# Performance work log

Measured on AMD Instinct MI355X. Metric: run time of the kernel, lower is better.

The kernel has to match this reference:

```python
import jax, jax.numpy as jnp
import numpy as np

N, E, C, H = 20000, 320000, 128, 8
DH = C // H
CUTOFF = 5.0
LN_EPS = 1e-5


def _xavier(k, fan_in, fan_out):
    lim = np.sqrt(6.0 / (fan_in + fan_out))
    return jax.random.uniform(k, (fan_in, fan_out), jnp.float32, -lim, lim)


def setup_inputs() -> dict:
    key = jax.random.key(0)
    ks = jax.random.split(key, 24)
    s = jax.random.normal(ks[0], (N, 1, C), jnp.float32)
    v = 0.1 * jax.random.normal(ks[1], (N, 3, C), jnp.float32)
    dir_ij = jax.random.normal(ks[2], (E, 3), jnp.float32)
    dir_ij = dir_ij / (jnp.linalg.norm(dir_ij, axis=-1, keepdims=True) + 1e-9)
    d_ij = jax.random.uniform(ks[3], (E,), jnp.float32, 0.0, CUTOFF)
    r_ij = 0.5 * jax.random.normal(ks[4], (E, C), jnp.float32)
    edge_index = jax.random.randint(ks[5], (2, E), 0, N, jnp.int64 if jax.config.jax_enable_x64 else jnp.int32)
    zb = lambda n: jnp.zeros((n,), jnp.float32)
    return {
        's': s, 'v': v, 'dir_ij': dir_ij, 'd_ij': d_ij, 'r_ij': r_ij,
        'edge_index': edge_index,
        'ln_g': jnp.ones((C,), jnp.float32), 'ln_b': zb(C),
        'Wq': _xavier(ks[6], C, C), 'bq': zb(C),
        'Wk': _xavier(ks[7], C, C), 'bk': zb(C),
        'Wg1': _xavier(ks[8], C, C), 'bg1': zb(C),
        'Wg2': _xavier(ks[9], C, 3 * C), 'bg2': zb(3 * C),
        'Wv1': _xavier(ks[10], C, C), 'bv1': zb(C),
        'Wv2': _xavier(ks[11], C, 3 * C), 'bv2': zb(3 * C),
        'Wre': _xavier(ks[12], C, C), 'bre': zb(C),
        'Wra': _xavier(ks[13], C, 3 * C), 'bra': zb(3 * C),
    }


def _layernorm(x, g, b):
    m = jnp.mean(x, axis=-1, keepdims=True)
    var = jnp.mean((x - m) ** 2, axis=-1, keepdims=True)
    return (x - m) * jax.lax.rsqrt(var + LN_EPS) * g + b


def _cosine_cutoff(d):
    return 0.5 * (jnp.cos(d * (np.pi / CUTOFF)) + 1.0) * (d < CUTOFF).astype(d.dtype)


def _segment_softmax(logits, seg, n):
    # logits: [E, H], seg: [E]
    m = jax.ops.segment_max(logits, seg, num_segments=n)
    m = jnp.where(jnp.isfinite(m), m, 0.0)
    e = jnp.exp(logits - m[seg])
    z = jax.ops.segment_sum(e, seg, num_segments=n)
    return e / (z[seg] + 1e-16)


def reference(s, v, dir_ij, d_ij, r_ij, edge_index,
              ln_g, ln_b, Wq, bq, Wk, bk, Wg1, bg1, Wg2, bg2,
              Wv1, bv1, Wv2, bv2, Wre, bre, Wra, bra):
    src, dst = edge_index[0], edge_index[1]  # PyG: x_j = x[src], x_i = x[dst]
    s_ln = _layernorm(s, ln_g, ln_b)          # [N,1,C]
    s2 = s_ln[:, 0, :]                         # [N,C]

    q = (s2 @ Wq + bq).reshape(N, H, DH)
    k = (s2 @ Wk + bk).reshape(N, H, DH)
    x3 = jax.nn.silu(s2 @ Wg1 + bg1) @ Wg2 + bg2   # gamma_s -> [N,3C]
    val = jax.nn.silu(s2 @ Wv1 + bv1) @ Wv2 + bv2  # gamma_v -> [N,3C]
    r_attn = jax.nn.silu(r_ij @ Wre + bre).reshape(E, H, DH)
    r_proj = r_ij @ Wra + bra                      # [E,3C]

    # attention logits and segment softmax over destination nodes
    alpha = jnp.einsum('ehd,ehd->eh', q[dst] * k[src], r_attn) if False else jnp.sum(q[dst] * k[src] * r_attn, axis=-1)  # [E,H]
    attn = _segment_softmax(alpha, dst, N)         # [E,H]

    sea = (attn[:, :, None] * val[src].reshape(E, H, 3 * DH)).reshape(E, 3 * C)
    saa = r_proj * x3[src] * _cosine_cutoff(d_ij)[:, None]
    msg = saa + sea                                # [E,3C]
    o_s, o_d, o_v = jnp.split(msg, 3, axis=-1)     # each [E,C]

    su = jax.ops.segment_sum(o_s, dst, num_segments=N)   # [N,C]
    v_msg = dir_ij[:, :, None] * o_d[:, None, :] + o_v[:, None, :] * v[src]  # [E,3,C]
    vu = jax.ops.segment_sum(v_msg, dst, num_segments=N)  # [N,3,C]

    s_out = s_ln + su[:, None, :]
    v_out = v + vu
    return s_out, v_out, r_ij  # last_layer=True returns f_ij unchanged
```

## Files before the change

kernel.cpp:

```cpp
#include <hip/hip_runtime.h>
#include <cstdint>
#include <cstddef>

#define N_NODES 20000
#define N_EDGES 320000

typedef __attribute__((ext_vector_type(8))) short short8;
typedef __attribute__((ext_vector_type(4))) float floatx4;

__device__ __forceinline__ unsigned short f2bf(float f){
  union { float f; unsigned int i; } v; v.f = f;
  unsigned int u = v.i;
  return (unsigned short)((u + 0x7FFFu + ((u >> 16) & 1u)) >> 16);
}
__device__ __forceinline__ float bf2f(unsigned short u){
  union { unsigned int i; float f; } v; v.i = ((unsigned int)u) << 16; return v.f;
}
__device__ __forceinline__ float siluf(float x){ return x / (1.f + __expf(-x)); }
__device__ __forceinline__ short8 ld_frag16(const unsigned short* p){
  uint4 u = *(const uint4*)p;
  return *(short8*)&u;
}
__device__ __forceinline__ int clampi(int x, int lo, int hi){ return min(max(x, lo), hi); }

__global__ void k_pack(const float* Wq, const float* Wk,
                       const float* Wg1, const float* Wv1,
                       const float* Wg2, const float* Wv2,
                       const float* Wre, const float* Wra,
                       const float* bq, const float* bk,
                       const float* bg1, const float* bv1,
                       const float* bg2, const float* bv2,
                       const float* bre, const float* bra,
                       unsigned short* B1p, unsigned short* Wg2p, unsigned short* Wv2p,
                       unsigned short* Wep,
                       float* bias1, float* biasg2, float* biasv2, float* biase,
                       int* hist)
{
  int tid = blockIdx.x * blockDim.x + threadIdx.x;
  if (tid < 229376){
    int idx, region;
    if (tid < 65536){ region = 0; idx = tid; }
    else if (tid < 114688){ region = 1; idx = tid - 65536; }
    else if (tid < 163840){ region = 2; idx = tid - 114688; }
    else { region = 3; idx = tid - 163840; }
    int j = idx & 7, lane = (idx >> 3) & 63, kk = (idx >> 9) & 3, c = idx >> 11;
    int k = kk*32 + (lane >> 4)*8 + j;
    int n = c*16 + (lane & 15);
    if (region == 0){
      float v = (n < 128) ? Wq[k*128 + n]
              : (n < 256) ? Wk[k*128 + n - 128]
              : (n < 384) ? Wg1[k*128 + n - 256]
              : Wv1[k*128 + n - 384];
      B1p[idx] = f2bf(v);
    } else if (region == 1){ Wg2p[idx] = f2bf(Wg2[k*384 + n]); }
    else if (region == 2){ Wv2p[idx] = f2bf(Wv2[k*384 + n]); }
    else {
      float v = (n < 128) ? Wre[k*128 + n] : Wra[k*384 + n - 128];
      Wep[idx] = f2bf(v);
    }
  }
  if (tid < 512){
    bias1[tid] = tid<128 ? bq[tid] : tid<256 ? bk[tid-128] : tid<384 ? bg1[tid-256] : bv1[tid-384];
    biase[tid] = tid<128 ? bre[tid] : bra[tid-128];
  }
  if (tid < 384){ biasg2[tid] = bg2[tid]; biasv2[tid] = bv2[tid]; }
  if (tid < N_NODES) hist[tid] = 0;
}

__global__ void k_ln(const float* s_in, const float* v_in, const float* g, const float* b,
                     unsigned short* s2b, unsigned short* vt)
{
  int wid = threadIdx.x >> 6, lane = threadIdx.x & 63;
  int n = blockIdx.x*4 + wid;
  if (n >= N_NODES) return;
  const float* row = s_in + (size_t)n*128;
  float2 xv = *(const float2*)(row + lane*2);
  float x0 = xv.x, x1 = xv.y;
  float s = x0 + x1, ss = x0*x0 + x1*x1;
  for (int m = 1; m <= 32; m <<= 1){ s += __shfl_xor(s, m); ss += __shfl_xor(ss, m); }
  float mean = s * (1.f/128.f);
  float var = ss * (1.f/128.f) - mean*mean;
  float rs = rsqrtf(var + 1e-5f);
  int ch = lane*2;
  float y0 = (x0-mean)*rs*g[ch]   + b[ch];
  float y1 = (x1-mean)*rs*g[ch+1] + b[ch+1];
  ushort2 ov; ov.x = f2bf(y0); ov.y = f2bf(y1);
  *(ushort2*)(s2b + (size_t)n*128 + ch) = ov;

  float2 va = *(const float2*)(v_in + ((size_t)n*3 + 0)*128 + ch);
  float2 vb = *(const float2*)(v_in + ((size_t)n*3 + 1)*128 + ch);
  float2 vc = *(const float2*)(v_in + ((size_t)n*3 + 2)*128 + ch);
  uint4 wv;
  wv.x = (unsigned int)f2bf(va.x) | ((unsigned int)f2bf(vb.x) << 16);
  wv.y = (unsigned int)f2bf(vc.x);
  wv.z = (unsigned int)f2bf(va.y) | ((unsigned int)f2bf(vb.y) << 16);
  wv.w = (unsigned int)f2bf(vc.y);
  *(uint4*)(vt + (size_t)n*512 + (size_t)ch*4) = wv;
}

__global__ void k_hist(const int* ei, int* hist){
  int e = blockIdx.x*blockDim.x + threadIdx.x;
  if (e < N_EDGES){
    int d = clampi(ei[N_EDGES + e], 0, N_NODES-1);
    atomicAdd(&hist[d], 1);
  }
}

__global__ void k_scan(const int* hist, int* row_start, int* cursor){
  __shared__ int wsum[17];
  __shared__ int carry_s;
  int tid = threadIdx.x, lane = tid & 63, wid = tid >> 6;
  if (tid == 0) carry_s = 0;
  __syncthreads();
  for (int base = 0; base < N_NODES; base += 1024){
    int i = base + tid;
    int v = (i < N_NODES) ? hist[i] : 0;
    int incl = v;
    for (int off = 1; off < 64; off <<= 1){
      int t = __shfl_up(incl, off);
      if (lane >= off) incl += t;
    }
    if (lane == 63) wsum[wid] = incl;
    __syncthreads();
    if (tid == 0){
      int acc = carry_s;
      for (int w2 = 0; w2 < 16; w2++){ int t = wsum[w2]; wsum[w2] = acc; acc += t; }
      wsum[16] = acc;
    }
    __syncthreads();
    int excl = wsum[wid] + incl - v;
    if (i < N_NODES){ row_start[i] = excl; cursor[i] = excl; }
    __syncthreads();
    if (tid == 0) carry_s = wsum[16];
    __syncthreads();
  }
  if (threadIdx.x == 0) row_start[N_NODES] = carry_s;
}

__global__ void k_scatter(const int* ei, const float* dir_ij, const float* d_ij,
                          int* cursor, int* perm_s, int* src_s, float* dird_s){
  int e = blockIdx.x*blockDim.x + threadIdx.x;
  if (e < N_EDGES){
    int d = clampi(ei[N_EDGES + e], 0, N_NODES-1);
    int pos = clampi(atomicAdd(&cursor[d], 1), 0, N_EDGES-1);
    perm_s[pos] = e;
    src_s[pos] = clampi(ei[e], 0, N_NODES-1);
    float4 dd;
    dd.x = dir_ij[(size_t)e*3 + 0];
    dd.y = dir_ij[(size_t)e*3 + 1];
    dd.z = dir_ij[(size_t)e*3 + 2];
    dd.w = d_ij[e];
    *(float4*)(dird_s + (size_t)pos*4) = dd;
  }
}

__global__ void __launch_bounds__(256) k_ngemm1(const unsigned short* s2b, const unsigned short* B1p, const float* bias1,
                        unsigned short* q_b, unsigned short* k_b, unsigned short* h1_b, unsigned short* h2_b)
{
  int wid = threadIdx.x >> 6, lane = threadIdx.x & 63;
  int tile = blockIdx.x*4 + wid;
  if (tile >= N_NODES/16) return;
  int l15 = lane & 15, q = lane >> 4;
  int n0 = tile*16;
  const unsigned short* arow = s2b + (size_t)(n0 + l15)*128 + q*8;
  short8 af[4];
  for (int kk = 0; kk < 4; kk++) af[kk] = ld_frag16(arow + kk*32);
  for (int c = 0; c < 32; c++){
    floatx4 acc = {0.f,0.f,0.f,0.f};
    const unsigned short* bp = B1p + (size_t)(c*4)*512 + lane*8;
    for (int kk = 0; kk < 4; kk++){
      short8 bf = ld_frag16(bp + kk*512);
      acc = __builtin_amdgcn_mfma_f32_16x16x32_bf16(af[kk], bf, acc, 0, 0, 0);
    }
    int col = c*16 + l15;
    float bias = bias1[col];
    unsigned short* dst; int cc;
    if      (c < 8){  dst = q_b;  cc = col; }
    else if (c < 16){ dst = k_b;  cc = col - 128; }
    else if (c < 24){ dst = h1_b; cc = col - 256; }
    else            { dst = h2_b; cc = col - 384; }
    bool act = (c >= 16);
    for (int r = 0; r < 4; r++){
      float vv = acc[r] + bias;
      if (act) vv = siluf(vv);
      int node = n0 + q*4 + r;
      dst[(size_t)node*128 + cc] = f2bf(vv);
    }
  }
}

__global__ void __launch_bounds__(256) k_ngemm2(const unsigned short* h1_b, const unsigned short* h2_b,
                        const unsigned short* Wg2p, const unsigned short* Wv2p,
                        const float* biasg2, const float* biasv2,
                        unsigned short* xv_b)
{
  int wid = threadIdx.x >> 6, lane = threadIdx.x & 63;
  int tile = blockIdx.x*4 + wid;
  if (tile >= N_NODES/16) return;
  int l15 = lane & 15, q = lane >> 4;
  int n0 = tile*16;
  for (int ph = 0; ph < 2; ph++){
    const unsigned short* srcm = ph ? h2_b : h1_b;
    const unsigned short* Wp   = ph ? Wv2p : Wg2p;
    const float* bs            = ph ? biasv2 : biasg2;
    const unsigned short* arow = srcm + (size_t)(n0 + l15)*128 + q*8;
    short8 af[4];
    for (int kk = 0; kk < 4; kk++) af[kk] = ld_frag16(arow + kk*32);
    for (int c = 0; c < 24; c++){
      floatx4 acc = {0.f,0.f,0.f,0.f};
      const unsigned short* bp = Wp + (size_t)(c*4)*512 + lane*8;
      for (int kk = 0; kk < 4; kk++){
        short8 bf = ld_frag16(bp + kk*512);
        acc = __builtin_amdgcn_mfma_f32_16x16x32_bf16(af[kk], bf, acc, 0, 0, 0);
      }
      int col = c*16 + l15;
      float bias = bs[col];
      for (int r = 0; r < 4; r++){
        float vv = acc[r] + bias;
        int node = n0 + q*4 + r;
        xv_b[(((size_t)node*384 + col) << 1) + ph] = f2bf(vv);
      }
    }
  }
}

__global__ void __launch_bounds__(256) k_alpha(const float* r_ij, const unsigned short* q_b, const unsigned short* k_b,
                       const unsigned short* Wep, const float* biase,
                       const int* row_start, const int* perm_s, const int* src_s,
                       float* alpha_s, float* stats_s, float* r_out)
{
  int wid = threadIdx.x >> 6, lane = threadIdx.x & 63;
  int n = blockIdx.x*4 + wid;
  int l15 = lane & 15, q = lane >> 4;
  int rs = clampi(row_start[n], 0, N_EDGES);
  int re = clampi(row_start[n+1], rs, N_EDGES);
  if (re <= rs) return;

  float m_run[8], z_run[8];
  #pragma unroll
  for (int h = 0; h < 8; h++){ m_run[h] = -1e30f; z_run[h] = 0.f; }

  for (int c0 = rs; c0 < re; c0 += 16){
    int iA = min(c0 + l15, re-1);
    bool validA = (c0 + l15 < re);
    int pA = clampi(perm_s[iA], 0, N_EDGES-1);
    const float* ar = r_ij + (size_t)pA*128 + q*8;
    float*       wr = r_out + (size_t)pA*128 + q*8;
    short8 af[4];
    for (int kk = 0; kk < 4; kk++){
      float4 a0 = *(const float4*)(ar + kk*32);
      float4 a1 = *(const float4*)(ar + kk*32 + 4);
      if (validA){ *(float4*)(wr + kk*32) = a0; *(float4*)(wr + kk*32 + 4) = a1; }
      short8 f;
      f[0]=(short)f2bf(a0.x); f[1]=(short)f2bf(a0.y); f[2]=(short)f2bf(a0.z); f[3]=(short)f2bf(a0.w);
      f[4]=(short)f2bf(a1.x); f[5]=(short)f2bf(a1.y); f[6]=(short)f2bf(a1.z); f[7]=(short)f2bf(a1.w);
      af[kk] = f;
    }
    int sv[4]; int er_[4]; bool vr[4];
    for (int r = 0; r < 4; r++){
      int e = c0 + q*4 + r;
      vr[r] = (e < re);
      int ec = min(e, re-1);
      er_[r] = e;
      sv[r] = clampi(src_s[ec], 0, N_NODES-1);
    }
    for (int c = 0; c < 8; c++){
      floatx4 acc = {0.f,0.f,0.f,0.f};
      const unsigned short* bp = Wep + (size_t)(c*4)*512 + lane*8;
      for (int kk = 0; kk < 4; kk++){
        short8 bf = ld_frag16(bp + kk*512);
        acc = __builtin_amdgcn_mfma_f32_16x16x32_bf16(af[kk], bf, acc, 0, 0, 0);
      }
      float bias = biase[c*16 + l15];
      float qv = bf2f(q_b[(size_t)n*128 + c*16 + l15]);
      float t0[4];
      for (int r = 0; r < 4; r++){
        float kvv = bf2f(k_b[(size_t)sv[r]*128 + c*16 + l15]);
        t0[r] = siluf(acc[r] + bias) * qv * kvv;
      }
      for (int m = 1; m <= 8; m <<= 1)
        for (int r = 0; r < 4; r++) t0[r] += __shfl_xor(t0[r], m);
      if (l15 == 0){
        for (int r = 0; r < 4; r++)
          if (vr[r]) alpha_s[(size_t)er_[r]*8 + c] = t0[r];
      }
      for (int r = 0; r < 4; r++){
        if (vr[r]){
          float t = t0[r];
          float mn = fmaxf(m_run[c], t);
          z_run[c] = z_run[c]*__expf(m_run[c]-mn) + __expf(t-mn);
          m_run[c] = mn;
        }
      }
    }
  }
  for (int h = 0; h < 8; h++){
    float mo = m_run[h], zo = z_run[h];
    for (int m = 16; m <= 32; m <<= 1){
      float m2 = __shfl_xor(mo, m), z2 = __shfl_xor(zo, m);
      float mn = fmaxf(mo, m2);
      zo = zo*__expf(mo-mn) + z2*__expf(m2-mn);
      mo = mn;
    }
    m_run[h] = mo; z_run[h] = zo;
  }
  if (lane == 0){
    for (int h = 0; h < 8; h++){
      stats_s[(size_t)n*16 + h]     = m_run[h];
      stats_s[(size_t)n*16 + 8 + h] = 1.f / (z_run[h] + 1e-16f);
    }
  }
}

__global__ void __launch_bounds__(256) k_msg(const float* s_in, const float* v_in,
                     const float* r_ij,
                     const float* ln_g, const float* ln_b,
                     const unsigned short* xv_b, const unsigned short* vt_b,
                     const unsigned short* Wep, const float* biase,
                     const int* row_start, const int* perm_s, const int* src_s,
                     const float* dird_s, const float* alpha_s, const float* stats_s,
                     float* out_s, float* out_v)
{
  int wid = threadIdx.x >> 6, lane = threadIdx.x & 63;
  int n = blockIdx.x*4 + wid;
  int l15 = lane & 15, q = lane >> 4;
  int rs = clampi(row_start[n], 0, N_EDGES);
  int re = clampi(row_start[n+1], rs, N_EDGES);

  float accS[2] = {0.f, 0.f};
  float accV[6] = {0.f,0.f,0.f,0.f,0.f,0.f};

  int lh = lane & 7;
  float mh = stats_s[(size_t)n*16 + lh];
  float zi = stats_s[(size_t)n*16 + 8 + lh];

  for (int c0 = rs; c0 < re; c0 += 16){
    int iA = min(c0 + l15, re-1);
    int pA = clampi(perm_s[iA], 0, N_EDGES-1);
    const float* ar = r_ij + (size_t)pA*128 + q*8;
    short8 af[4];
    for (int kk = 0; kk < 4; kk++){
      float4 a0 = *(const float4*)(ar + kk*32);
      float4 a1 = *(const float4*)(ar + kk*32 + 4);
      short8 f;
      f[0]=(short)f2bf(a0.x); f[1]=(short)f2bf(a0.y); f[2]=(short)f2bf(a0.z); f[3]=(short)f2bf(a0.w);
      f[4]=(short)f2bf(a1.x); f[5]=(short)f2bf(a1.y); f[6]=(short)f2bf(a1.z); f[7]=(short)f2bf(a1.w);
      af[kk] = f;
    }

    int sv[4]; int er_[4]; bool vr[4]; float cc[4], dv0[4], dv1[4], dv2[4];
    for (int r = 0; r < 4; r++){
      int e = c0 + q*4 + r;
      vr[r] = (e < re);
      int ec = min(e, re-1);
      er_[r] = ec;
      sv[r] = clampi(src_s[ec], 0, N_NODES-1);
      float4 dd = *(const float4*)(dird_s + (size_t)ec*4);
      cc[r] = (vr[r] && dd.w < 5.0f) ? 0.5f*(__cosf(dd.w*0.6283185307179587f) + 1.f) : 0.f;
      dv0[r] = dd.x; dv1[r] = dd.y; dv2[r] = dd.z;
    }

    float at4[4] = {0.f,0.f,0.f,0.f};
    for (int c = 0; c < 24; c++){
      if (c % 3 == 0){
        int h = c / 3;
        float mhc = __shfl(mh, h);
        float zic = __shfl(zi, h);
        for (int r = 0; r < 4; r++)
          at4[r] = vr[r] ? __expf(alpha_s[(size_t)er_[r]*8 + h] - mhc) * zic : 0.f;
      }
      floatx4 acc = {0.f,0.f,0.f,0.f};
      const unsigned short* bp = Wep + (size_t)((8+c)*4)*512 + lane*8;
      for (int kk = 0; kk < 4; kk++){
        short8 bf = ld_frag16(bp + kk*512);
        acc = __builtin_amdgcn_mfma_f32_16x16x32_bf16(af[kk], bf, acc, 0, 0, 0);
      }
      float bias = biase[128 + c*16 + l15];
      float msg[4];
      for (int r = 0; r < 4; r++){
        unsigned int xv = *(const unsigned int*)(xv_b + (((size_t)sv[r]*384 + c*16 + l15) << 1));
        float xvf = bf2f((unsigned short)(xv & 0xffffu));
        float vvf = bf2f((unsigned short)(xv >> 16));
        msg[r] = (acc[r] + bias) * xvf * cc[r] + at4[r] * vvf;
      }
      if (c < 8){
        float s4 = msg[0]+msg[1]+msg[2]+msg[3];
        s4 += __shfl_xor(s4, 16); s4 += __shfl_xor(s4, 32);
        if (q == (c & 3)) accS[c >> 2] += s4;
      } else if (c < 16){
        int b = c - 8;
        float p0 = msg[0]*dv0[0] + msg[1]*dv0[1] + msg[2]*dv0[2] + msg[3]*dv0[3];
        float p1 = msg[0]*dv1[0] + msg[1]*dv1[1] + msg[2]*dv1[2] + msg[3]*dv1[3];
        float p2 = msg[0]*dv2[0] + msg[1]*dv2[1] + msg[2]*dv2[2] + msg[3]*dv2[3];
        p0 += __shfl_xor(p0, 16); p0 += __shfl_xor(p0, 32);
        p1 += __shfl_xor(p1, 16); p1 += __shfl_xor(p1, 32);
        p2 += __shfl_xor(p2, 16); p2 += __shfl_xor(p2, 32);
        if (q == (b & 3)){
          accV[(b >> 2)*3 + 0] += p0;
          accV[(b >> 2)*3 + 1] += p1;
          accV[(b >> 2)*3 + 2] += p2;
        }
      } else {
        int b = c - 16;
        float p0 = 0.f, p1 = 0.f, p2 = 0.f;
        for (int r = 0; r < 4; r++){
          uint2 vv = *(const uint2*)(vt_b + (((size_t)sv[r]*128 + b*16 + l15) << 2));
          p0 += msg[r] * bf2f((unsigned short)(vv.x & 0xffffu));
          p1 += msg[r] * bf2f((unsigned short)(vv.x >> 16));
          p2 += msg[r] * bf2f((unsigned short)(vv.y & 0xffffu));
        }
        p0 += __shfl_xor(p0, 16); p0 += __shfl_xor(p0, 32);
        p1 += __shfl_xor(p1, 16); p1 += __shfl_xor(p1, 32);
        p2 += __shfl_xor(p2, 16); p2 += __shfl_xor(p2, 32);
        if (q == (b & 3)){
          accV[(b >> 2)*3 + 0] += p0;
          accV[(b >> 2)*3 + 1] += p1;
          accV[(b >> 2)*3 + 2] += p2;
        }
      }
    }
  }

  {
    int ch0 = q*16 + l15, ch1 = 64 + q*16 + l15;
    float x0 = s_in[(size_t)n*128 + ch0];
    float x1 = s_in[(size_t)n*128 + ch1];
    float sm = x0 + x1, ssq = x0*x0 + x1*x1;
    for (int m = 1; m <= 32; m <<= 1){ sm += __shfl_xor(sm, m); ssq += __shfl_xor(ssq, m); }
    float mean = sm * (1.f/128.f);
    float var = ssq * (1.f/128.f) - mean*mean;
    float rsv = rsqrtf(var + 1e-5f);
    float y0 = (x0-mean)*rsv*ln_g[ch0] + ln_b[ch0];
    float y1 = (x1-mean)*rsv*ln_g[ch1] + ln_b[ch1];
    out_s[(size_t)n*128 + ch0] = y0 + accS[0];
    out_s[(size_t)n*128 + ch1] = y1 + accS[1];
  }
  for (int t = 0; t < 6; t++){
    int b = (t/3)*4 + q;
    int a = t - (t/3)*3;
    int ch = b*16 + l15;
    size_t idx = ((size_t)n*3 + a)*128 + ch;
    out_v[idx] = v_in[idx] + accV[t];
  }
}

extern "C" void kernel_launch(void* const* d_in, const int* in_sizes, int n_in,
                              void* d_out, int out_size, void* d_ws, size_t ws_size,
                              hipStream_t stream)
{
  const float* s_in   = (const float*)d_in[0];
  const float* v_in   = (const float*)d_in[1];
  const float* dir_ij = (const float*)d_in[2];
  const float* d_ij   = (const float*)d_in[3];
  const float* r_ij   = (const float*)d_in[4];
  const int*   ei     = (const int*)d_in[5];
  const float* ln_g   = (const float*)d_in[6];
  const float* ln_b   = (const float*)d_in[7];
  const float* Wq  = (const float*)d_in[8];
  const float* bq  = (const float*)d_in[9];
  const float* Wk  = (const float*)d_in[10];
  const float* bk  = (const float*)d_in[11];
  const float* Wg1 = (const float*)d_in[12];
  const float* bg1 = (const float*)d_in[13];
  const float* Wg2 = (const float*)d_in[14];
  const float* bg2 = (const float*)d_in[15];
  const float* Wv1 = (const float*)d_in[16];
  const float* bv1 = (const float*)d_in[17];
  const float* Wv2 = (const float*)d_in[18];
  const float* bv2 = (const float*)d_in[19];
  const float* Wre = (const float*)d_in[20];
  const float* bre = (const float*)d_in[21];
  const float* Wra = (const float*)d_in[22];
  const float* bra = (const float*)d_in[23];

  float* out_s = (float*)d_out;
  float* out_v = out_s + (size_t)N_NODES*128;
  float* out_r = out_v + (size_t)N_NODES*384;

  char* w = (char*)d_ws;
  size_t off = 0;
  auto alloc = [&](size_t bytes) -> void* {
    void* p = w + off;
    off = (off + bytes + 255) & ~(size_t)255;
    return p;
  };
  char* reg0 = (char*)alloc((size_t)N_EDGES*8*4);
  unsigned short* h1_b  = (unsigned short*)reg0;
  unsigned short* h2_b  = (unsigned short*)(reg0 + (size_t)N_NODES*128*2);
  float* alpha_s        = (float*)reg0;
  unsigned short* xv_b  = (unsigned short*)alloc((size_t)N_NODES*384*2*2);
  unsigned short* s2b   = xv_b;
  unsigned short* q_b   = (unsigned short*)alloc((size_t)N_NODES*128*2);
  unsigned short* k_b   = (unsigned short*)alloc((size_t)N_NODES*128*2);
  unsigned short* vt_b  = (unsigned short*)alloc((size_t)N_NODES*128*4*2);
  float* dird_s  = (float*)alloc((size_t)N_EDGES*4*4);
  float* stats_s = (float*)alloc((size_t)N_NODES*16*4);
  unsigned short* B1p   = (unsigned short*)alloc(65536*2);
  unsigned short* Wg2p  = (unsigned short*)alloc(49152*2);
  unsigned short* Wv2p  = (unsigned short*)alloc(49152*2);
  unsigned short* Wep   = (unsigned short*)alloc(65536*2);
  float* bias1  = (float*)alloc(512*4);
  float* biasg2 = (float*)alloc(384*4);
  float* biasv2 = (float*)alloc(384*4);
  float* biase  = (float*)alloc(512*4);
  int* hist      = (int*)alloc((size_t)N_NODES*4);
  int* row_start = (int*)alloc((size_t)(N_NODES+1)*4);
  int* cursor    = (int*)alloc((size_t)N_NODES*4);
  int* perm_s    = (int*)alloc((size_t)N_EDGES*4);
  int* src_s     = (int*)alloc((size_t)N_EDGES*4);

  k_pack<<<896, 256, 0, stream>>>(Wq, Wk, Wg1, Wv1, Wg2, Wv2, Wre, Wra,
                                  bq, bk, bg1, bv1, bg2, bv2, bre, bra,
                                  B1p, Wg2p, Wv2p, Wep,
                                  bias1, biasg2, biasv2, biase, hist);
  k_ln<<<5000, 256, 0, stream>>>(s_in, v_in, ln_g, ln_b, s2b, vt_b);
  k_hist<<<1250, 256, 0, stream>>>(ei, hist);
  k_scan<<<1, 1024, 0, stream>>>(hist, row_start, cursor);
  k_scatter<<<1250, 256, 0, stream>>>(ei, dir_ij, d_ij, cursor, perm_s, src_s, dird_s);
  k_ngemm1<<<313, 256, 0, stream>>>(s2b, B1p, bias1, q_b, k_b, h1_b, h2_b);
  k_ngemm2<<<313, 256, 0, stream>>>(h1_b, h2_b, Wg2p, Wv2p, biasg2, biasv2, xv_b);
  k_alpha<<<5000, 256, 0, stream>>>(r_ij, q_b, k_b, Wep, biase, row_start, perm_s, src_s,
                                    alpha_s, stats_s, out_r);
  k_msg<<<5000, 256, 0, stream>>>(s_in, v_in, r_ij, ln_g, ln_b,
                                  xv_b, vt_b, Wep, biase,
                                  row_start, perm_s, src_s, dird_s, alpha_s, stats_s,
                                  out_s, out_v);
}
```

Before: 1.021 ms.

## Cache bf16 edge features in sorted order and re-layout gathered node table

k_alpha now also writes a bf16 copy of r_ij in destination-sorted order, and k_msg reads it contiguously instead of re-gathering the fp32 rows through perm_s and converting them again. This halves the edge-feature bytes read in k_msg and removes the random gather, at the cost of an extra write pass and an 82 MB workspace buffer. The xv_b table is re-laid out so the 24 column chunks per lane are contiguous, which lets k_msg fetch four chunks per source node with one 16-byte load instead of many 4-byte gathers. The fallback path depends on the workspace size check.

```diff
diff --git a/kernel.cpp b/kernel.cpp
--- a/kernel.cpp
+++ b/kernel.cpp
@@ -218,13 +218,14 @@
       for (int r = 0; r < 4; r++){
         float vv = acc[r] + bias;
         int node = n0 + q*4 + r;
-        xv_b[(((size_t)node*384 + col) << 1) + ph] = f2bf(vv);
-      }
-    }
-  }
-}
-
-__global__ void __launch_bounds__(256) k_alpha(const float* r_ij, const unsigned short* q_b, const unsigned short* k_b,
+        xv_b[((((size_t)node*16 + l15)*24 + c) << 1) + ph] = f2bf(vv);
+      }
+    }
+  }
+}
+
+__global__ void __launch_bounds__(256) k_alpha(const float* r_ij, unsigned short* r_srt, int use_srt,
+                       const unsigned short* q_b, const unsigned short* k_b,
                        const unsigned short* Wep, const float* biase,
                        const int* row_start, const int* perm_s, const int* src_s,
                        float* alpha_s, float* stats_s, float* r_out)
@@ -246,6 +247,7 @@
     int pA = clampi(perm_s[iA], 0, N_EDGES-1);
     const float* ar = r_ij + (size_t)pA*128 + q*8;
     float*       wr = r_out + (size_t)pA*128 + q*8;
+    unsigned short* wsrt = r_srt + (size_t)iA*128 + q*8;
     short8 af[4];
     for (int kk = 0; kk < 4; kk++){
       float4 a0 = *(const float4*)(ar + kk*32);
@@ -255,6 +257,7 @@
       f[0]=(short)f2bf(a0.x); f[1]=(short)f2bf(a0.y); f[2]=(short)f2bf(a0.z); f[3]=(short)f2bf(a0.w);
       f[4]=(short)f2bf(a1.x); f[5]=(short)f2bf(a1.y); f[6]=(short)f2bf(a1.z); f[7]=(short)f2bf(a1.w);
       af[kk] = f;
+      if (use_srt && validA) *(short8*)(wsrt + kk*32) = f;
     }
     int sv[4]; int er_[4]; bool vr[4];
     for (int r = 0; r < 4; r++){
@@ -313,7 +316,7 @@
 }
 
 __global__ void __launch_bounds__(256) k_msg(const float* s_in, const float* v_in,
-                     const float* r_ij,
+                     const float* r_ij, const unsigned short* r_srt, int use_srt,
                      const float* ln_g, const float* ln_b,
                      const unsigned short* xv_b, const unsigned short* vt_b,
                      const unsigned short* Wep, const float* biase,
@@ -336,19 +339,25 @@
 
   for (int c0 = rs; c0 < re; c0 += 16){
     int iA = min(c0 + l15, re-1);
-    int pA = clampi(perm_s[iA], 0, N_EDGES-1);
-    const float* ar = r_ij + (size_t)pA*128 + q*8;
     short8 af[4];
-    for (int kk = 0; kk < 4; kk++){
-      float4 a0 = *(const float4*)(ar + kk*32);
-      float4 a1 = *(const float4*)(ar + kk*32 + 4);
-      short8 f;
-      f[0]=(short)f2bf(a0.x); f[1]=(short)f2bf(a0.y); f[2]=(short)f2bf(a0.z); f[3]=(short)f2bf(a0.w);
-      f[4]=(short)f2bf(a1.x); f[5]=(short)f2bf(a1.y); f[6]=(short)f2bf(a1.z); f[7]=(short)f2bf(a1.w);
-      af[kk] = f;
+    if (use_srt){
+      const unsigned short* ar = r_srt + (size_t)iA*128 + q*8;
+      for (int kk = 0; kk < 4; kk++) af[kk] = ld_frag16(ar + kk*32);
+    } else {
+      int pA = clampi(perm_s[iA], 0, N_EDGES-1);
+      const float* ar = r_ij + (size_t)pA*128 + q*8;
+      for (int kk = 0; kk < 4; kk++){
+        float4 a0 = *(const float4*)(ar + kk*32);
+        float4 a1 = *(const float4*)(ar + kk*32 + 4);
+        short8 f;
+        f[0]=(short)f2bf(a0.x); f[1]=(short)f2bf(a0.y); f[2]=(short)f2bf(a0.z); f[3]=(short)f2bf(a0.w);
+        f[4]=(short)f2bf(a1.x); f[5]=(short)f2bf(a1.y); f[6]=(short)f2bf(a1.z); f[7]=(short)f2bf(a1.w);
+        af[kk] = f;
+      }
     }
 
     int sv[4]; int er_[4]; bool vr[4]; float cc[4], dv0[4], dv1[4], dv2[4];
+    #pragma unroll
     for (int r = 0; r < 4; r++){
       int e = c0 + q*4 + r;
       vr[r] = (e < re);
@@ -361,61 +370,75 @@
     }
 
     float at4[4] = {0.f,0.f,0.f,0.f};
-    for (int c = 0; c < 24; c++){
-      if (c % 3 == 0){
-        int h = c / 3;
-        float mhc = __shfl(mh, h);
-        float zic = __shfl(zi, h);
-        for (int r = 0; r < 4; r++)
-          at4[r] = vr[r] ? __expf(alpha_s[(size_t)er_[r]*8 + h] - mhc) * zic : 0.f;
-      }
-      floatx4 acc = {0.f,0.f,0.f,0.f};
-      const unsigned short* bp = Wep + (size_t)((8+c)*4)*512 + lane*8;
-      for (int kk = 0; kk < 4; kk++){
-        short8 bf = ld_frag16(bp + kk*512);
-        acc = __builtin_amdgcn_mfma_f32_16x16x32_bf16(af[kk], bf, acc, 0, 0, 0);
-      }
-      float bias = biase[128 + c*16 + l15];
-      float msg[4];
-      for (int r = 0; r < 4; r++){
-        unsigned int xv = *(const unsigned int*)(xv_b + (((size_t)sv[r]*384 + c*16 + l15) << 1));
-        float xvf = bf2f((unsigned short)(xv & 0xffffu));
-        float vvf = bf2f((unsigned short)(xv >> 16));
-        msg[r] = (acc[r] + bias) * xvf * cc[r] + at4[r] * vvf;
-      }
-      if (c < 8){
-        float s4 = msg[0]+msg[1]+msg[2]+msg[3];
-        s4 += __shfl_xor(s4, 16); s4 += __shfl_xor(s4, 32);
-        if (q == (c & 3)) accS[c >> 2] += s4;
-      } else if (c < 16){
-        int b = c - 8;
-        float p0 = msg[0]*dv0[0] + msg[1]*dv0[1] + msg[2]*dv0[2] + msg[3]*dv0[3];
-        float p1 = msg[0]*dv1[0] + msg[1]*dv1[1] + msg[2]*dv1[2] + msg[3]*dv1[3];
-        float p2 = msg[0]*dv2[0] + msg[1]*dv2[1] + msg[2]*dv2[2] + msg[3]*dv2[3];
-        p0 += __shfl_xor(p0, 16); p0 += __shfl_xor(p0, 32);
-        p1 += __shfl_xor(p1, 16); p1 += __shfl_xor(p1, 32);
-        p2 += __shfl_xor(p2, 16); p2 += __shfl_xor(p2, 32);
-        if (q == (b & 3)){
-          accV[(b >> 2)*3 + 0] += p0;
-          accV[(b >> 2)*3 + 1] += p1;
-          accV[(b >> 2)*3 + 2] += p2;
+    #pragma unroll 1
+    for (int gc = 0; gc < 6; gc++){
+      uint4 Xr0 = *(const uint4*)(xv_b + ((((size_t)sv[0]*16 + l15)*24 + gc*4) << 1));
+      uint4 Xr1 = *(const uint4*)(xv_b + ((((size_t)sv[1]*16 + l15)*24 + gc*4) << 1));
+      uint4 Xr2 = *(const uint4*)(xv_b + ((((size_t)sv[2]*16 + l15)*24 + gc*4) << 1));
+      uint4 Xr3 = *(const uint4*)(xv_b + ((((size_t)sv[3]*16 + l15)*24 + gc*4) << 1));
+      #pragma unroll
+      for (int j = 0; j < 4; j++){
+        int c = gc*4 + j;
+        if (c % 3 == 0){
+          int h = c / 3;
+          float mhc = __shfl(mh, h);
+          float zic = __shfl(zi, h);
+          #pragma unroll
+          for (int r = 0; r < 4; r++)
+            at4[r] = vr[r] ? __expf(alpha_s[(size_t)er_[r]*8 + h] - mhc) * zic : 0.f;
         }
-      } else {
-        int b = c - 16;
-        float p0 = 0.f, p1 = 0.f, p2 = 0.f;
-        for (int r = 0; r < 4; r++){
-          uint2 vv = *(const uint2*)(vt_b + (((size_t)sv[r]*128 + b*16 + l15) << 2));
-          p0 += msg[r] * bf2f((unsigned short)(vv.x & 0xffffu));
-          p1 += msg[r] * bf2f((unsigned short)(vv.x >> 16));
-          p2 += msg[r] * bf2f((unsigned short)(vv.y & 0xffffu));
+        floatx4 acc = {0.f,0.f,0.f,0.f};
+        const unsigned short* bp = Wep + (size_t)((8+c)*4)*512 + lane*8;
+        #pragma unroll
+        for (int kk = 0; kk < 4; kk++){
+          short8 bf = ld_frag16(bp + kk*512);
+          acc = __builtin_amdgcn_mfma_f32_16x16x32_bf16(af[kk], bf, acc, 0, 0, 0);
         }
-        p0 += __shfl_xor(p0, 16); p0 += __shfl_xor(p0, 32);
-        p1 += __shfl_xor(p1, 16); p1 += __shfl_xor(p1, 32);
-        p2 += __shfl_xor(p2, 16); p2 += __shfl_xor(p2, 32);
-        if (q == (b & 3)){
-          accV[(b >> 2)*3 + 0] += p0;
-          accV[(b >> 2)*3 + 1] += p1;
-          accV[(b >> 2)*3 + 2] += p2;
+        float bias = biase[128 + c*16 + l15];
+        unsigned int xu0 = (j==0)?Xr0.x:(j==1)?Xr0.y:(j==2)?Xr0.z:Xr0.w;
+        unsigned int xu1 = (j==0)?Xr1.x:(j==1)?Xr1.y:(j==2)?Xr1.z:Xr1.w;
+        unsigned int xu2 = (j==0)?Xr2.x:(j==1)?Xr2.y:(j==2)?Xr2.z:Xr2.w;
+        unsigned int xu3 = (j==0)?Xr3.x:(j==1)?Xr3.y:(j==2)?Xr3.z:Xr3.w;
+        float msg[4];
+        msg[0] = (acc[0] + bias) * bf2f((unsigned short)(xu0 & 0xffffu)) * cc[0] + at4[0] * bf2f((unsigned short)(xu0 >> 16));
+        msg[1] = (acc[1] + bias) * bf2f((unsigned short)(xu1 & 0xffffu)) * cc[1] + at4[1] * bf2f((unsigned short)(xu1 >> 16));
+        msg[2] = (acc[2] + bias) * bf2f((unsigned short)(xu2 & 0xffffu)) * cc[2] + at4[2] * bf2f((unsigned short)(xu2 >> 16));
+        msg[3] = (acc[3] + bias) * bf2f((unsigned short)(xu3 & 0xffffu)) * cc[3] + at4[3] * bf2f((unsigned short)(xu3 >> 16));
+        if (c < 8){
+          float s4 = msg[0]+msg[1]+msg[2]+msg[3];
+          s4 += __shfl_xor(s4, 16); s4 += __shfl_xor(s4, 32);
+          if (q == (c & 3)) accS[c >> 2] += s4;
+        } else if (c < 16){
+          int b = c - 8;
+          float p0 = msg[0]*dv0[0] + msg[1]*dv0[1] + msg[2]*dv0[2] + msg[3]*dv0[3];
+          float p1 = msg[0]*dv1[0] + msg[1]*dv1[1] + msg[2]*dv1[2] + msg[3]*dv1[3];
+          float p2 = msg[0]*dv2[0] + msg[1]*dv2[1] + msg[2]*dv2[2] + msg[3]*dv2[3];
+          p0 += __shfl_xor(p0, 16); p0 += __shfl_xor(p0, 32);
+          p1 += __shfl_xor(p1, 16); p1 += __shfl_xor(p1, 32);
+          p2 += __shfl_xor(p2, 16); p2 += __shfl_xor(p2, 32);
+          if (q == (b & 3)){
+            accV[(b >> 2)*3 + 0] += p0;
+            accV[(b >> 2)*3 + 1] += p1;
+            accV[(b >> 2)*3 + 2] += p2;
+          }
+        } else {
+          int b = c - 16;
+          float p0 = 0.f, p1 = 0.f, p2 = 0.f;
+          #pragma unroll
+          for (int r = 0; r < 4; r++){
+            uint2 vv = *(const uint2*)(vt_b + (((size_t)sv[r]*128 + b*16 + l15) << 2));
+            p0 += msg[r] * bf2f((unsigned short)(vv.x & 0xffffu));
+            p1 += msg[r] * bf2f((unsigned short)(vv.x >> 16));
+            p2 += msg[r] * bf2f((unsigned short)(vv.y & 0xffffu));
+          }
+          p0 += __shfl_xor(p0, 16); p0 += __shfl_xor(p0, 32);
+          p1 += __shfl_xor(p1, 16); p1 += __shfl_xor(p1, 32);
+          p2 += __shfl_xor(p2, 16); p2 += __shfl_xor(p2, 32);
+          if (q == (b & 3)){
+            accV[(b >> 2)*3 + 0] += p0;
+            accV[(b >> 2)*3 + 1] += p1;
+            accV[(b >> 2)*3 + 2] += p2;
+          }
         }
       }
     }
@@ -508,6 +531,8 @@
   int* cursor    = (int*)alloc((size_t)N_NODES*4);
   int* perm_s    = (int*)alloc((size_t)N_EDGES*4);
   int* src_s     = (int*)alloc((size_t)N_EDGES*4);
+  unsigned short* r_srt = (unsigned short*)alloc((size_t)N_EDGES*128*2);
+  int use_srt = (off <= ws_size) ? 1 : 0;
 
   k_pack<<<896, 256, 0, stream>>>(Wq, Wk, Wg1, Wv1, Wg2, Wv2, Wre, Wra,
                                   bq, bk, bg1, bv1, bg2, bv2, bre, bra,
@@ -519,9 +544,9 @@
   k_scatter<<<1250, 256, 0, stream>>>(ei, dir_ij, d_ij, cursor, perm_s, src_s, dird_s);
   k_ngemm1<<<313, 256, 0, stream>>>(s2b, B1p, bias1, q_b, k_b, h1_b, h2_b);
   k_ngemm2<<<313, 256, 0, stream>>>(h1_b, h2_b, Wg2p, Wv2p, biasg2, biasv2, xv_b);
-  k_alpha<<<5000, 256, 0, stream>>>(r_ij, q_b, k_b, Wep, biase, row_start, perm_s, src_s,
-                                    alpha_s, stats_s, out_r);
-  k_msg<<<5000, 256, 0, stream>>>(s_in, v_in, r_ij, ln_g, ln_b,
+  k_alpha<<<5000, 256, 0, stream>>>(r_ij, r_srt, use_srt, q_b, k_b, Wep, biase,
+                                    row_start, perm_s, src_s, alpha_s, stats_s, out_r);
+  k_msg<<<5000, 256, 0, stream>>>(s_in, v_in, r_ij, r_srt, use_srt, ln_g, ln_b,
                                   xv_b, vt_b, Wep, biase,
                                   row_start, perm_s, src_s, dird_s, alpha_s, stats_s,
                                   out_s, out_v);
```

New measurement: 1.491 ms. 1.46x slower.
